# Performance work log

Measured on AMD Instinct MI355X. Metric: run time of the kernel, lower is better.

Reference implementation:

```python
import jax, jax.numpy as jnp
import numpy as np

B, T, C = 4, 1024, 768
E, K = 8, 2               # n_exp, top_k
N = B * T                 # num_tokens
# eval-mode capacity: floor(K * eval_capacity(2.0) * N / E), rounded even, >= min_capacity(4)
CAP = 2048


def setup_inputs() -> dict:
    key = jax.random.key(0)
    k0, k1, k2, k3 = jax.random.split(key, 4)
    s = 0.02
    return {
        "x": jax.random.normal(k0, (B, T, C), jnp.float32),
        "w_g": jax.random.normal(k1, (E, C), jnp.float32) * s,
        "c_fc": jax.random.normal(k2, (E, C, 4 * C), jnp.float32) * s,
        "fc_bias": jnp.zeros((E, 1, 4 * C), jnp.float32),
        "c_proj": jax.random.normal(k3, (E, 4 * C, C), jnp.float32) * s,
        "proj_bias": jnp.zeros((E, 1, C), jnp.float32),
    }


def reference(x, w_g, c_fc, fc_bias, c_proj, proj_bias):
    xf = x.reshape(N, C)
    # ---- Router ----
    logits = xf @ w_g.T                                        # [N, E]
    top_v, top_i = jax.lax.top_k(logits, K)                    # [N, K]
    rows = jnp.arange(N)[:, None]
    masked = jnp.full((N, E), -jnp.inf, logits.dtype).at[rows, top_i].set(top_v)
    probs = jax.nn.softmax(masked, axis=-1)                    # [N, E] (zero off top-k)
    exp_mask = jax.nn.one_hot(top_i, E, dtype=jnp.float32)     # [N, K, E]
    exp_mask = exp_mask.transpose(1, 0, 2)                     # [K, N, E]
    # position of each assignment within its expert queue (top-1 assignments first)
    rank = jnp.cumsum(exp_mask.reshape(K * N, E), axis=0) - 1.0
    rank = rank.reshape(K, N, E)
    exp_mask = exp_mask * (rank < CAP)                         # drop over-capacity tokens
    rank_id = jnp.sum(exp_mask * rank, axis=-1).astype(jnp.int32)  # [K, N]
    exp_w = exp_mask * probs[None]                             # [K, N, E]
    rank_sc = jax.nn.one_hot(rank_id, CAP, dtype=jnp.float32)  # [K, N, CAP]
    cb_weight = jnp.einsum('kne,knc->nec', exp_w, rank_sc)     # [N, E, CAP] combine weights
    sec_mask = (cb_weight != 0).astype(xf.dtype)               # [N, E, CAP] dispatch mask
    # ---- Dispatch + batched experts (per-expert MLP via bmm) ----
    exp_in = jnp.einsum('nec,nd->ecd', sec_mask, xf)           # [E, CAP, C]
    h = jax.nn.gelu(jnp.einsum('ecd,edf->ecf', exp_in, c_fc) + fc_bias, approximate=False)
    exp_out = jnp.einsum('ecf,efd->ecd', h, c_proj) + proj_bias  # [E, CAP, C]
    # ---- Combine ----
    out = jnp.einsum('nec,ecd->nd', cb_weight, exp_out)        # [N, C]
    return out.reshape(B, T, C)
```

## Files before the change

### kernel.cpp

```cpp
#include <hip/hip_runtime.h>
#include <hip/hip_bf16.h>
#include <math.h>

#define N_TOK 4096
#define CDIM  768
#define E_EXP 8
#define CAPC  2048
#define HDIM  3072

typedef __attribute__((ext_vector_type(8))) short short8;
typedef __attribute__((ext_vector_type(4))) float floatx4;

#define VMCNT(n) asm volatile("s_waitcnt vmcnt(" #n ")" ::: "memory")
#define LGKM(n)  asm volatile("s_waitcnt lgkmcnt(" #n ")" ::: "memory")
#define SB0()    __builtin_amdgcn_sched_barrier(0)

static __device__ __forceinline__ unsigned short f2bf(float f) {
  __hip_bfloat16 h = __float2bfloat16(f);
  return __builtin_bit_cast(unsigned short, h);
}
static __device__ __forceinline__ float bf2f(unsigned short u) {
  return __builtin_bit_cast(float, (unsigned int)u << 16);
}

__global__ __launch_bounds__(256)
void transpose64(const float* __restrict__ in, __hip_bfloat16* __restrict__ out,
                 int R, int Cc)
{
  __shared__ float tile[64][65];
  const int e  = blockIdx.z;
  const int c0 = blockIdx.x * 64;
  const int r0 = blockIdx.y * 64;
  const float* ie = in + (size_t)e * R * Cc;
  unsigned short* oe = (unsigned short*)out + (size_t)e * Cc * R;
  const int t = threadIdx.x;
  {
    const int r = t >> 2, c = (t & 3) * 4;
#pragma unroll
    for (int i = 0; i < 4; ++i) {
      const float4 v = *(const float4*)(ie + (size_t)(r0 + r) * Cc + c0 + c + i * 16);
      tile[r][c + i * 16 + 0] = v.x; tile[r][c + i * 16 + 1] = v.y;
      tile[r][c + i * 16 + 2] = v.z; tile[r][c + i * 16 + 3] = v.w;
    }
  }
  __syncthreads();
  {
    const int cc = t >> 2, rq = (t & 3) * 16;
    unsigned short o[16];
#pragma unroll
    for (int i = 0; i < 16; ++i) o[i] = f2bf(tile[rq + i][cc]);
    unsigned short* dst = oe + (size_t)(c0 + cc) * R + r0 + rq;
    *(short8*)(dst)     = *(short8*)&o[0];
    *(short8*)(dst + 8) = *(short8*)&o[8];
  }
}

__global__ __launch_bounds__(256)
void router_kernel(const float* __restrict__ x, const float* __restrict__ wg,
                   int* __restrict__ eidx, float* __restrict__ pval)
{
  const int wv = threadIdx.x >> 6, lane = threadIdx.x & 63;
  const int n = blockIdx.x * 4 + wv;
  const float* xr = x + (size_t)n * CDIM;
  float acc[E_EXP] = {0.f, 0.f, 0.f, 0.f, 0.f, 0.f, 0.f, 0.f};
#pragma unroll
  for (int i = 0; i < CDIM / 64; ++i) {
    const float xv = xr[i * 64 + lane];
#pragma unroll
    for (int e = 0; e < E_EXP; ++e)
      acc[e] = fmaf(xv, wg[e * CDIM + i * 64 + lane], acc[e]);
  }
#pragma unroll
  for (int e = 0; e < E_EXP; ++e) {
#pragma unroll
    for (int off = 32; off > 0; off >>= 1)
      acc[e] += __shfl_xor(acc[e], off);
  }
  if (lane == 0) {
    int e0 = 0; float v0 = acc[0];
#pragma unroll
    for (int e = 1; e < E_EXP; ++e) if (acc[e] > v0) { v0 = acc[e]; e0 = e; }
    int e1 = -1; float v1 = -3.4e38f;
#pragma unroll
    for (int e = 0; e < E_EXP; ++e) if (e != e0 && acc[e] > v1) { v1 = acc[e]; e1 = e; }
    const float ex = __expf(v1 - v0);
    const float inv = 1.f / (1.f + ex);
    eidx[n] = e0; eidx[N_TOK + n] = e1;
    pval[n] = inv; pval[N_TOK + n] = ex * inv;
  }
}

__global__ __launch_bounds__(256)
void scan_kernel(const int* __restrict__ eidx, int* __restrict__ slot,
                 int* __restrict__ slot_token, int* __restrict__ ecnt,
                 int* __restrict__ work2, int* __restrict__ wcnt)
{
  const int t = threadIdx.x;
  const int base = t * 32;
  int e_local[32];
  int cnt[E_EXP] = {0, 0, 0, 0, 0, 0, 0, 0};
#pragma unroll
  for (int i = 0; i < 32; ++i) {
    const int e = eidx[base + i];
    e_local[i] = e;
    cnt[e]++;
  }
  __shared__ int hist[256][E_EXP];
  __shared__ int secnt[E_EXP];
#pragma unroll
  for (int e = 0; e < E_EXP; ++e) hist[t][e] = cnt[e];
  __syncthreads();
  for (int off = 1; off < 256; off <<= 1) {
    int v[E_EXP] = {0, 0, 0, 0, 0, 0, 0, 0};
    if (t >= off) {
#pragma unroll
      for (int e = 0; e < E_EXP; ++e) v[e] = hist[t - off][e];
    }
    __syncthreads();
    if (t >= off) {
#pragma unroll
      for (int e = 0; e < E_EXP; ++e) hist[t][e] += v[e];
    }
    __syncthreads();
  }
  if (t == 255) {
#pragma unroll
    for (int e = 0; e < E_EXP; ++e) {
      const int tot = hist[255][e];
      const int c = tot < CAPC ? tot : CAPC;
      ecnt[e] = c;
      secnt[e] = c;
    }
  }
  __syncthreads();
  if (t == 0) {
    int n2 = 0;
    for (int e = 0; e < E_EXP; ++e) {
      const int c = secnt[e];
      const int t2 = (c + 127) >> 7;
      for (int b = 0; b < t2; ++b) work2[n2++] = (e << 8) | b;
    }
    wcnt[0] = n2 * 24;
    wcnt[1] = n2 * 6;
  }
  int run[E_EXP];
#pragma unroll
  for (int e = 0; e < E_EXP; ++e) run[e] = hist[t][e] - cnt[e];
#pragma unroll
  for (int i = 0; i < 32; ++i) {
    const int a = base + i;
    const int e = e_local[i];
    const int r = run[e]++;
    const int s = (r < CAPC) ? r : -1;
    slot[a] = s;
    if (s >= 0) slot_token[e * CAPC + s] = (a < N_TOK) ? a : (a - N_TOK);
  }
}

__global__ __launch_bounds__(256)
void dispatch_kernel(const float* __restrict__ x, const int* __restrict__ slot_token,
                     const int* __restrict__ ecnt, __hip_bfloat16* __restrict__ xin)
{
  const int wv = threadIdx.x >> 6, lane = threadIdx.x & 63;
  const int s = blockIdx.x * 4 + wv;
  const int e = s >> 11;
  if ((s & (CAPC - 1)) >= ecnt[e]) return;
  const int n = slot_token[s];
  unsigned short* orow = (unsigned short*)xin + (size_t)s * CDIM;
  const float4* xr = (const float4*)(x + (size_t)n * CDIM);
#pragma unroll
  for (int i = 0; i < 3; ++i) {
    const float4 v = xr[i * 64 + lane];
    ushort4 o;
    o.x = f2bf(v.x); o.y = f2bf(v.y); o.z = f2bf(v.z); o.w = f2bf(v.w);
    *(ushort4*)(orow + (size_t)(i * 64 + lane) * 4) = o;
  }
}

__device__ __forceinline__ void stage_ab(const __hip_bfloat16* Ae, const __hip_bfloat16* Be,
                                         char* lds, int K, int kt, int isB,
                                         int wv, int lane)
{
  const char* src = (const char*)(isB ? Be : Ae);
  char* dst = lds + (kt & 1) * 32768 + isB * 16384;
#pragma unroll
  for (int j = 0; j < 4; ++j) {
    const int li = j * 32 + wv * 8 + (lane >> 3);
    const int kb = ((lane & 7) * 16) ^ ((li & 7) << 4);
    const char* g = src + ((size_t)li * K + (size_t)kt * 64) * 2 + kb;
    char* lp = dst + j * 4096 + wv * 1024;
    __builtin_amdgcn_global_load_lds((const __attribute__((address_space(1))) unsigned int*)g,
                                     (__attribute__((address_space(3))) unsigned int*)lp, 16, 0, 0);
  }
}

template<int VME, bool S2>
__device__ __forceinline__ void ktile2(int kt, char* lds,
                                       const __hip_bfloat16* Ae, const __hip_bfloat16* Be,
                                       int K, floatx4 (&acc)[4][4],
                                       int wm, int wn, int fr, int fk, int wv, int lane)
{
  if constexpr (VME == 8) VMCNT(8); else VMCNT(0);
  __builtin_amdgcn_s_barrier();
  SB0();
  const char* bufA = lds + ((kt & 1) ? 32768 : 0);
  const char* bufB = bufA + 16384;
  short8 a[4][2], b[4][2];
#pragma unroll
  for (int mi = 0; mi < 4; ++mi) {
    const int lr = wm * 64 + mi * 16 + fr;
    a[mi][0] = *(const short8*)(bufA + lr * 128 + ((fk * 16) ^ ((lr & 7) << 4)));
  }
#pragma unroll
  for (int ni = 0; ni < 4; ++ni) {
    const int lj = wn * 64 + ni * 16 + fr;
    b[ni][0] = *(const short8*)(bufB + lj * 128 + ((fk * 16) ^ ((lj & 7) << 4)));
  }
  SB0();
#pragma unroll
  for (int mi = 0; mi < 4; ++mi) {
    const int lr = wm * 64 + mi * 16 + fr;
    a[mi][1] = *(const short8*)(bufA + lr * 128 + ((64 + fk * 16) ^ ((lr & 7) << 4)));
  }
#pragma unroll
  for (int ni = 0; ni < 4; ++ni) {
    const int lj = wn * 64 + ni * 16 + fr;
    b[ni][1] = *(const short8*)(bufB + lj * 128 + ((64 + fk * 16) ^ ((lj & 7) << 4)));
  }
  SB0();
  LGKM(8); SB0();
  __builtin_amdgcn_s_setprio(1);
#pragma unroll
  for (int mi = 0; mi < 4; ++mi)
#pragma unroll
    for (int ni = 0; ni < 4; ++ni)
      acc[mi][ni] = __builtin_amdgcn_mfma_f32_16x16x32_bf16(a[mi][0], b[ni][0], acc[mi][ni], 0, 0, 0);
  __builtin_amdgcn_s_setprio(0);
  SB0();
  LGKM(0); SB0();
  __builtin_amdgcn_s_setprio(1);
#pragma unroll
  for (int mi = 0; mi < 4; ++mi)
#pragma unroll
    for (int ni = 0; ni < 4; ++ni)
      acc[mi][ni] = __builtin_amdgcn_mfma_f32_16x16x32_bf16(a[mi][1], b[ni][1], acc[mi][ni], 0, 0, 0);
  __builtin_amdgcn_s_setprio(0);
  SB0();
  __builtin_amdgcn_s_barrier();
  if (S2) {
    stage_ab(Ae, Be, lds, K, kt + 2, 0, wv, lane);
    stage_ab(Ae, Be, lds, K, kt + 2, 1, wv, lane);
  }
  SB0();
}

static __device__ __forceinline__ float gelu_fast(float v) {
  const float u2 = v * (1.5957691216f + 0.0713548163f * v * v);
  const float ez = __expf(u2);
  return v * ez / (ez + 1.0f);
}

template<int EPI, int NBX2, int WSEL>
__global__ __launch_bounds__(256, 2)
void gemm2x(const __hip_bfloat16* __restrict__ A, const __hip_bfloat16* __restrict__ Bt,
            const float* __restrict__ bias, __hip_bfloat16* __restrict__ Cout,
            int Nn, int K,
            const int* __restrict__ work, const int* __restrict__ wcnt)
{
  extern __shared__ __align__(16) char lds[];
  const int T = wcnt[WSEL];
  const int bId = blockIdx.x;
  const int cpx = (T + 7) >> 3;
  if ((bId >> 3) >= cpx) return;
  const int idx = (bId & 7) * cpx + (bId >> 3);
  if (idx >= T) return;
  const int p = idx / NBX2;
  const int bx0 = idx % NBX2;
  const int bx = (p & 1) ? (NBX2 - 1 - bx0) : bx0;
  const int w = work[p];
  const int e = w >> 8, by = w & 255;

  const int t = threadIdx.x, wv = t >> 6, lane = t & 63;
  const int wm = wv >> 1, wn = wv & 1;
  const int fr = lane & 15, fk = lane >> 4;
  const int ntk = K >> 6;

  const __hip_bfloat16* Ae = A + (size_t)e * CAPC * K + (size_t)by * 128 * K;
  const __hip_bfloat16* Be = Bt + (size_t)e * Nn * K + (size_t)bx * 128 * K;

  floatx4 acc[4][4] = {};

  stage_ab(Ae, Be, lds, K, 0, 0, wv, lane);
  stage_ab(Ae, Be, lds, K, 0, 1, wv, lane);
  stage_ab(Ae, Be, lds, K, 1, 0, wv, lane);
  stage_ab(Ae, Be, lds, K, 1, 1, wv, lane);
  SB0();

  for (int kt = 0; kt < ntk - 2; ++kt)
    ktile2<8, true>(kt, lds, Ae, Be, K, acc, wm, wn, fr, fk, wv, lane);
  ktile2<8, false>(ntk - 2, lds, Ae, Be, K, acc, wm, wn, fr, fk, wv, lane);
  ktile2<0, false>(ntk - 1, lds, Ae, Be, K, acc, wm, wn, fr, fk, wv, lane);

  const float* be = bias + (size_t)e * Nn;
  unsigned short* Cb = (unsigned short*)Cout + (size_t)e * CAPC * Nn;
  const int m0 = by * 128, n0 = bx * 128;
  unsigned short* ep = (unsigned short*)(lds + wv * 2048);
  float bcol[4];
#pragma unroll
  for (int ni = 0; ni < 4; ++ni) bcol[ni] = be[n0 + wn * 64 + ni * 16 + fr];
#pragma unroll
  for (int mi = 0; mi < 4; ++mi) {
#pragma unroll
    for (int ni = 0; ni < 4; ++ni)
#pragma unroll
      for (int j = 0; j < 4; ++j) {
        float v = acc[mi][ni][j] + bcol[ni];
        if (EPI == 1) v = gelu_fast(v);
        const int row = fk * 4 + j;
        *(unsigned short*)((char*)ep + row * 128 + ((ni * 32 + fr * 2) ^ (fk << 5))) = f2bf(v);
      }
    LGKM(0); SB0();
    const int r = lane & 15;
    const int grow = m0 + wm * 64 + mi * 16 + r;
#pragma unroll
    for (int it = 0; it < 2; ++it) {
      const int q = (lane >> 4) + it * 4;
      const short8 vv = *(const short8*)((char*)ep + r * 128 + ((q * 16) ^ ((r >> 2) << 5)));
      *(short8*)(Cb + (size_t)grow * Nn + n0 + wn * 64 + q * 8) = vv;
    }
    LGKM(0); SB0();
  }
}

__global__ __launch_bounds__(256)
void combine_kernel(const __hip_bfloat16* __restrict__ eout, const int* __restrict__ eidx,
                    const float* __restrict__ pval, const int* __restrict__ slot,
                    float* __restrict__ out)
{
  const int wv = threadIdx.x >> 6, lane = threadIdx.x & 63;
  const int n = blockIdx.x * 4 + wv;
  const int e0 = eidx[n], e1 = eidx[N_TOK + n];
  int s0 = slot[n], s1 = slot[N_TOK + n];
  const float w0 = (s0 >= 0) ? pval[n] : 0.f;
  const float w1 = (s1 >= 0) ? pval[N_TOK + n] : 0.f;
  s0 = (s0 >= 0) ? s0 : 0;
  s1 = (s1 >= 0) ? s1 : 0;
  const ushort4* r0 = (const ushort4*)((const unsigned short*)eout + ((size_t)e0 * CAPC + s0) * CDIM);
  const ushort4* r1 = (const ushort4*)((const unsigned short*)eout + ((size_t)e1 * CAPC + s1) * CDIM);
  float4* o = (float4*)(out + (size_t)n * CDIM);
#pragma unroll
  for (int i = 0; i < 3; ++i) {
    const ushort4 a = r0[i * 64 + lane];
    const ushort4 b = r1[i * 64 + lane];
    float4 c;
    c.x = w0 * bf2f(a.x) + w1 * bf2f(b.x);
    c.y = w0 * bf2f(a.y) + w1 * bf2f(b.y);
    c.z = w0 * bf2f(a.z) + w1 * bf2f(b.z);
    c.w = w0 * bf2f(a.w) + w1 * bf2f(b.w);
    o[i * 64 + lane] = c;
  }
}

extern "C" void kernel_launch(void* const* d_in, const int* in_sizes, int n_in,
                              void* d_out, int out_size, void* d_ws, size_t ws_size,
                              hipStream_t stream)
{
  const float* x   = (const float*)d_in[0];
  const float* wg  = (const float*)d_in[1];
  const float* cfc = (const float*)d_in[2];
  const float* fcb = (const float*)d_in[3];
  const float* cpr = (const float*)d_in[4];
  const float* prb = (const float*)d_in[5];
  float* out = (float*)d_out;

  char* ws = (char*)d_ws;
  size_t off = 0;
  auto take = [&](size_t bytes) -> void* {
    void* p = ws + off;
    off += (bytes + 255) & ~(size_t)255;
    return p;
  };
  __hip_bfloat16* wfcT = (__hip_bfloat16*)take((size_t)E_EXP * HDIM * CDIM * 2);
  __hip_bfloat16* wprT = (__hip_bfloat16*)take((size_t)E_EXP * CDIM * HDIM * 2);
  __hip_bfloat16* xin  = (__hip_bfloat16*)take((size_t)E_EXP * CAPC * CDIM * 2);
  __hip_bfloat16* hbuf = (__hip_bfloat16*)take((size_t)E_EXP * CAPC * HDIM * 2);
  __hip_bfloat16* eout = (__hip_bfloat16*)take((size_t)E_EXP * CAPC * CDIM * 2);
  int*   eidx = (int*)take((size_t)2 * N_TOK * 4);
  float* pv   = (float*)take((size_t)2 * N_TOK * 4);
  int*   slot = (int*)take((size_t)2 * N_TOK * 4);
  int*   stok = (int*)take((size_t)E_EXP * CAPC * 4);
  int*   ecnt = (int*)take((size_t)E_EXP * 4);
  int*   work2 = (int*)take((size_t)128 * 4);
  int*   wcnt = (int*)take((size_t)2 * 4);

  hipFuncSetAttribute((const void*)gemm2x<1, 24, 0>,
                      hipFuncAttributeMaxDynamicSharedMemorySize, 65536);
  hipFuncSetAttribute((const void*)gemm2x<2, 6, 1>,
                      hipFuncAttributeMaxDynamicSharedMemorySize, 65536);

  transpose64<<<dim3(HDIM / 64, CDIM / 64, E_EXP), 256, 0, stream>>>(cfc, wfcT, CDIM, HDIM);
  transpose64<<<dim3(CDIM / 64, HDIM / 64, E_EXP), 256, 0, stream>>>(cpr, wprT, HDIM, CDIM);

  router_kernel<<<N_TOK / 4, 256, 0, stream>>>(x, wg, eidx, pv);
  scan_kernel<<<1, 256, 0, stream>>>(eidx, slot, stok, ecnt, work2, wcnt);
  dispatch_kernel<<<(E_EXP * CAPC) / 4, 256, 0, stream>>>(x, stok, ecnt, xin);

  gemm2x<1, 24, 0><<<3072, 256, 65536, stream>>>(xin, wfcT, fcb, hbuf, HDIM, CDIM, work2, wcnt);
  gemm2x<2, 6, 1><<<768, 256, 65536, stream>>>(hbuf, wprT, prb, eout, CDIM, HDIM, work2, wcnt);

  combine_kernel<<<N_TOK / 4, 256, 0, stream>>>(eout, eidx, pv, slot, out);
}
```

Measured before the change: 185.9 us.

## Fuse transposes and router into one launch; make first GEMM persistent

Merges the two weight transposes and the router into a single prep kernel to cut launch overhead and let the pieces overlap. The first expert GEMM becomes a persistent kernel with 512 blocks, each looping over tiles with a stride of 64, instead of 3072 one-shot blocks. Both GEMMs now hardcode their dimensions as constants and mark the k-loop unroll 1. The persistent loop adds a barrier between tiles and may balance load worse across the CUs.

```diff
diff --git a/kernel.cpp b/kernel.cpp
--- a/kernel.cpp
+++ b/kernel.cpp
@@ -23,16 +23,11 @@
   return __builtin_bit_cast(float, (unsigned int)u << 16);
 }
 
-__global__ __launch_bounds__(256)
-void transpose64(const float* __restrict__ in, __hip_bfloat16* __restrict__ out,
-                 int R, int Cc)
-{
-  __shared__ float tile[64][65];
-  const int e  = blockIdx.z;
-  const int c0 = blockIdx.x * 64;
-  const int r0 = blockIdx.y * 64;
-  const float* ie = in + (size_t)e * R * Cc;
-  unsigned short* oe = (unsigned short*)out + (size_t)e * Cc * R;
+__device__ __forceinline__ void transpose_body(const float* __restrict__ ie,
+                                               unsigned short* __restrict__ oe,
+                                               int R, int Cc, int c0, int r0,
+                                               float (*tile)[65])
+{
   const int t = threadIdx.x;
   {
     const int r = t >> 2, c = (t & 3) * 4;
@@ -56,37 +51,56 @@
 }
 
 __global__ __launch_bounds__(256)
-void router_kernel(const float* __restrict__ x, const float* __restrict__ wg,
-                   int* __restrict__ eidx, float* __restrict__ pval)
-{
-  const int wv = threadIdx.x >> 6, lane = threadIdx.x & 63;
-  const int n = blockIdx.x * 4 + wv;
-  const float* xr = x + (size_t)n * CDIM;
-  float acc[E_EXP] = {0.f, 0.f, 0.f, 0.f, 0.f, 0.f, 0.f, 0.f};
-#pragma unroll
-  for (int i = 0; i < CDIM / 64; ++i) {
-    const float xv = xr[i * 64 + lane];
-#pragma unroll
-    for (int e = 0; e < E_EXP; ++e)
-      acc[e] = fmaf(xv, wg[e * CDIM + i * 64 + lane], acc[e]);
-  }
-#pragma unroll
-  for (int e = 0; e < E_EXP; ++e) {
-#pragma unroll
-    for (int off = 32; off > 0; off >>= 1)
-      acc[e] += __shfl_xor(acc[e], off);
-  }
-  if (lane == 0) {
-    int e0 = 0; float v0 = acc[0];
-#pragma unroll
-    for (int e = 1; e < E_EXP; ++e) if (acc[e] > v0) { v0 = acc[e]; e0 = e; }
-    int e1 = -1; float v1 = -3.4e38f;
-#pragma unroll
-    for (int e = 0; e < E_EXP; ++e) if (e != e0 && acc[e] > v1) { v1 = acc[e]; e1 = e; }
-    const float ex = __expf(v1 - v0);
-    const float inv = 1.f / (1.f + ex);
-    eidx[n] = e0; eidx[N_TOK + n] = e1;
-    pval[n] = inv; pval[N_TOK + n] = ex * inv;
+void prep_kernel(const float* __restrict__ cfc, const float* __restrict__ cpr,
+                 __hip_bfloat16* __restrict__ wfcT, __hip_bfloat16* __restrict__ wprT,
+                 const float* __restrict__ x, const float* __restrict__ wg,
+                 int* __restrict__ eidx, float* __restrict__ pval)
+{
+  __shared__ float tile[64][65];
+  const int b = blockIdx.x;
+  if (b < 4608) {
+    const int e = b / (48 * 12), rem = b % (48 * 12);
+    const int c0 = (rem % 48) * 64, r0 = (rem / 48) * 64;
+    transpose_body(cfc + (size_t)e * CDIM * HDIM,
+                   (unsigned short*)wfcT + (size_t)e * HDIM * CDIM,
+                   CDIM, HDIM, c0, r0, tile);
+  } else if (b < 9216) {
+    const int bb = b - 4608;
+    const int e = bb / (12 * 48), rem = bb % (12 * 48);
+    const int c0 = (rem % 12) * 64, r0 = (rem / 12) * 64;
+    transpose_body(cpr + (size_t)e * HDIM * CDIM,
+                   (unsigned short*)wprT + (size_t)e * CDIM * HDIM,
+                   HDIM, CDIM, c0, r0, tile);
+  } else {
+    const int wv = threadIdx.x >> 6, lane = threadIdx.x & 63;
+    const int n = (b - 9216) * 4 + wv;
+    const float* xr = x + (size_t)n * CDIM;
+    float acc[E_EXP] = {0.f, 0.f, 0.f, 0.f, 0.f, 0.f, 0.f, 0.f};
+#pragma unroll
+    for (int i = 0; i < CDIM / 64; ++i) {
+      const float xv = xr[i * 64 + lane];
+#pragma unroll
+      for (int e = 0; e < E_EXP; ++e)
+        acc[e] = fmaf(xv, wg[e * CDIM + i * 64 + lane], acc[e]);
+    }
+#pragma unroll
+    for (int e = 0; e < E_EXP; ++e) {
+#pragma unroll
+      for (int off = 32; off > 0; off >>= 1)
+        acc[e] += __shfl_xor(acc[e], off);
+    }
+    if (lane == 0) {
+      int e0 = 0; float v0 = acc[0];
+#pragma unroll
+      for (int e = 1; e < E_EXP; ++e) if (acc[e] > v0) { v0 = acc[e]; e0 = e; }
+      int e1 = -1; float v1 = -3.4e38f;
+#pragma unroll
+      for (int e = 0; e < E_EXP; ++e) if (e != e0 && acc[e] > v1) { v1 = acc[e]; e1 = e; }
+      const float ex = __expf(v1 - v0);
+      const float inv = 1.f / (1.f + ex);
+      eidx[n] = e0; eidx[N_TOK + n] = e1;
+      pval[n] = inv; pval[N_TOK + n] = ex * inv;
+    }
   }
 }
 
@@ -260,50 +274,13 @@
   return v * ez / (ez + 1.0f);
 }
 
-template<int EPI, int NBX2, int WSEL>
-__global__ __launch_bounds__(256, 2)
-void gemm2x(const __hip_bfloat16* __restrict__ A, const __hip_bfloat16* __restrict__ Bt,
-            const float* __restrict__ bias, __hip_bfloat16* __restrict__ Cout,
-            int Nn, int K,
-            const int* __restrict__ work, const int* __restrict__ wcnt)
-{
-  extern __shared__ __align__(16) char lds[];
-  const int T = wcnt[WSEL];
-  const int bId = blockIdx.x;
-  const int cpx = (T + 7) >> 3;
-  if ((bId >> 3) >= cpx) return;
-  const int idx = (bId & 7) * cpx + (bId >> 3);
-  if (idx >= T) return;
-  const int p = idx / NBX2;
-  const int bx0 = idx % NBX2;
-  const int bx = (p & 1) ? (NBX2 - 1 - bx0) : bx0;
-  const int w = work[p];
-  const int e = w >> 8, by = w & 255;
-
-  const int t = threadIdx.x, wv = t >> 6, lane = t & 63;
-  const int wm = wv >> 1, wn = wv & 1;
-  const int fr = lane & 15, fk = lane >> 4;
-  const int ntk = K >> 6;
-
-  const __hip_bfloat16* Ae = A + (size_t)e * CAPC * K + (size_t)by * 128 * K;
-  const __hip_bfloat16* Be = Bt + (size_t)e * Nn * K + (size_t)bx * 128 * K;
-
-  floatx4 acc[4][4] = {};
-
-  stage_ab(Ae, Be, lds, K, 0, 0, wv, lane);
-  stage_ab(Ae, Be, lds, K, 0, 1, wv, lane);
-  stage_ab(Ae, Be, lds, K, 1, 0, wv, lane);
-  stage_ab(Ae, Be, lds, K, 1, 1, wv, lane);
-  SB0();
-
-  for (int kt = 0; kt < ntk - 2; ++kt)
-    ktile2<8, true>(kt, lds, Ae, Be, K, acc, wm, wn, fr, fk, wv, lane);
-  ktile2<8, false>(ntk - 2, lds, Ae, Be, K, acc, wm, wn, fr, fk, wv, lane);
-  ktile2<0, false>(ntk - 1, lds, Ae, Be, K, acc, wm, wn, fr, fk, wv, lane);
-
-  const float* be = bias + (size_t)e * Nn;
-  unsigned short* Cb = (unsigned short*)Cout + (size_t)e * CAPC * Nn;
-  const int m0 = by * 128, n0 = bx * 128;
+template<int EPI>
+__device__ __forceinline__ void epilogue_bf16(floatx4 (&acc)[4][4], char* lds,
+                                              const float* be, unsigned short* Cb,
+                                              int Nn, int m0, int n0,
+                                              int wm, int wn, int fr, int fk,
+                                              int wv, int lane)
+{
   unsigned short* ep = (unsigned short*)(lds + wv * 2048);
   float bcol[4];
 #pragma unroll
@@ -330,6 +307,101 @@
     }
     LGKM(0); SB0();
   }
+}
+
+__global__ __launch_bounds__(256, 2)
+void gemm1p(const __hip_bfloat16* __restrict__ A, const __hip_bfloat16* __restrict__ Bt,
+            const float* __restrict__ bias, __hip_bfloat16* __restrict__ Cout,
+            const int* __restrict__ work, const int* __restrict__ wcnt)
+{
+  extern __shared__ __align__(16) char lds[];
+  const int T = wcnt[0];
+  const int cpx = (T + 7) >> 3;
+  const int x8 = blockIdx.x & 7, l = blockIdx.x >> 3;
+  const int lim = (x8 + 1) * cpx < T ? (x8 + 1) * cpx : T;
+
+  const int t = threadIdx.x, wv = t >> 6, lane = t & 63;
+  const int wm = wv >> 1, wn = wv & 1;
+  const int fr = lane & 15, fk = lane >> 4;
+  constexpr int ntk = CDIM / 64;
+
+  for (int i = x8 * cpx + l; i < lim; i += 64) {
+    const int p = i / 24;
+    const int bx0 = i % 24;
+    const int bx = (p & 1) ? (23 - bx0) : bx0;
+    const int w = work[p];
+    const int e = w >> 8, by = w & 255;
+
+    const __hip_bfloat16* Ae = A + (size_t)e * CAPC * CDIM + (size_t)by * 128 * CDIM;
+    const __hip_bfloat16* Be = Bt + (size_t)e * HDIM * CDIM + (size_t)bx * 128 * CDIM;
+
+    floatx4 acc[4][4] = {};
+
+    stage_ab(Ae, Be, lds, CDIM, 0, 0, wv, lane);
+    stage_ab(Ae, Be, lds, CDIM, 0, 1, wv, lane);
+    stage_ab(Ae, Be, lds, CDIM, 1, 0, wv, lane);
+    stage_ab(Ae, Be, lds, CDIM, 1, 1, wv, lane);
+    SB0();
+
+#pragma unroll 1
+    for (int kt = 0; kt < ntk - 2; ++kt)
+      ktile2<8, true>(kt, lds, Ae, Be, CDIM, acc, wm, wn, fr, fk, wv, lane);
+    ktile2<8, false>(ntk - 2, lds, Ae, Be, CDIM, acc, wm, wn, fr, fk, wv, lane);
+    ktile2<0, false>(ntk - 1, lds, Ae, Be, CDIM, acc, wm, wn, fr, fk, wv, lane);
+
+    epilogue_bf16<1>(acc, lds,
+                     bias + (size_t)e * HDIM,
+                     (unsigned short*)Cout + (size_t)e * CAPC * HDIM,
+                     HDIM, by * 128, bx * 128, wm, wn, fr, fk, wv, lane);
+    __builtin_amdgcn_s_barrier();
+    SB0();
+  }
+}
+
+__global__ __launch_bounds__(256, 2)
+void gemm2x(const __hip_bfloat16* __restrict__ A, const __hip_bfloat16* __restrict__ Bt,
+            const float* __restrict__ bias, __hip_bfloat16* __restrict__ Cout,
+            const int* __restrict__ work, const int* __restrict__ wcnt)
+{
+  extern __shared__ __align__(16) char lds[];
+  const int T = wcnt[1];
+  const int bId = blockIdx.x;
+  const int cpx = (T + 7) >> 3;
+  if ((bId >> 3) >= cpx) return;
+  const int idx = (bId & 7) * cpx + (bId >> 3);
+  if (idx >= T) return;
+  const int p = idx / 6;
+  const int bx0 = idx % 6;
+  const int bx = (p & 1) ? (5 - bx0) : bx0;
+  const int w = work[p];
+  const int e = w >> 8, by = w & 255;
+
+  const int t = threadIdx.x, wv = t >> 6, lane = t & 63;
+  const int wm = wv >> 1, wn = wv & 1;
+  const int fr = lane & 15, fk = lane >> 4;
+  constexpr int ntk = HDIM / 64;
+
+  const __hip_bfloat16* Ae = A + (size_t)e * CAPC * HDIM + (size_t)by * 128 * HDIM;
+  const __hip_bfloat16* Be = Bt + (size_t)e * CDIM * HDIM + (size_t)bx * 128 * HDIM;
+
+  floatx4 acc[4][4] = {};
+
+  stage_ab(Ae, Be, lds, HDIM, 0, 0, wv, lane);
+  stage_ab(Ae, Be, lds, HDIM, 0, 1, wv, lane);
+  stage_ab(Ae, Be, lds, HDIM, 1, 0, wv, lane);
+  stage_ab(Ae, Be, lds, HDIM, 1, 1, wv, lane);
+  SB0();
+
+#pragma unroll 1
+  for (int kt = 0; kt < ntk - 2; ++kt)
+    ktile2<8, true>(kt, lds, Ae, Be, HDIM, acc, wm, wn, fr, fk, wv, lane);
+  ktile2<8, false>(ntk - 2, lds, Ae, Be, HDIM, acc, wm, wn, fr, fk, wv, lane);
+  ktile2<0, false>(ntk - 1, lds, Ae, Be, HDIM, acc, wm, wn, fr, fk, wv, lane);
+
+  epilogue_bf16<2>(acc, lds,
+                   bias + (size_t)e * CDIM,
+                   (unsigned short*)Cout + (size_t)e * CAPC * CDIM,
+                   CDIM, by * 128, bx * 128, wm, wn, fr, fk, wv, lane);
 }
 
 __global__ __launch_bounds__(256)
@@ -393,20 +465,18 @@
   int*   work2 = (int*)take((size_t)128 * 4);
   int*   wcnt = (int*)take((size_t)2 * 4);
 
-  hipFuncSetAttribute((const void*)gemm2x<1, 24, 0>,
+  hipFuncSetAttribute((const void*)gemm1p,
                       hipFuncAttributeMaxDynamicSharedMemorySize, 65536);
-  hipFuncSetAttribute((const void*)gemm2x<2, 6, 1>,
+  hipFuncSetAttribute((const void*)gemm2x,
                       hipFuncAttributeMaxDynamicSharedMemorySize, 65536);
 
-  transpose64<<<dim3(HDIM / 64, CDIM / 64, E_EXP), 256, 0, stream>>>(cfc, wfcT, CDIM, HDIM);
-  transpose64<<<dim3(CDIM / 64, HDIM / 64, E_EXP), 256, 0, stream>>>(cpr, wprT, HDIM, CDIM);
-
-  router_kernel<<<N_TOK / 4, 256, 0, stream>>>(x, wg, eidx, pv);
+  prep_kernel<<<4608 + 4608 + 1024, 256, 0, stream>>>(cfc, cpr, wfcT, wprT,
+                                                      x, wg, eidx, pv);
   scan_kernel<<<1, 256, 0, stream>>>(eidx, slot, stok, ecnt, work2, wcnt);
   dispatch_kernel<<<(E_EXP * CAPC) / 4, 256, 0, stream>>>(x, stok, ecnt, xin);
 
-  gemm2x<1, 24, 0><<<3072, 256, 65536, stream>>>(xin, wfcT, fcb, hbuf, HDIM, CDIM, work2, wcnt);
-  gemm2x<2, 6, 1><<<768, 256, 65536, stream>>>(hbuf, wprT, prb, eout, CDIM, HDIM, work2, wcnt);
+  gemm1p<<<512, 256, 65536, stream>>>(xin, wfcT, fcb, hbuf, work2, wcnt);
+  gemm2x<<<768, 256, 65536, stream>>>(hbuf, wprT, prb, eout, work2, wcnt);
 
   combine_kernel<<<N_TOK / 4, 256, 0, stream>>>(eout, eidx, pv, slot, out);
 }
```

Measured after the change: 175.4 us. -5.7%, faster.
